# Optimization experiments

Measured on AMD Instinct MI355X. Metric: run time of the kernel, lower is better.

The kernel has to match this reference:

```python
import jax, jax.numpy as jnp
import numpy as np

B, W, E, D, F = 128, 64, 256, 256, 4  # batch, window, enc_hidden, dec_hidden, out_feats


def setup_inputs() -> dict:
    key = jax.random.key(0)
    ks = jax.random.split(key, 16)
    s = 0.05
    return {
        "input_encoded": jax.random.normal(ks[0], (B, W, E), jnp.float32),
        "y_history": jax.random.normal(ks[1], (B, W, F), jnp.float32),
        # attn_layer: Linear(2D+E -> E), Tanh, Linear(E -> 1)
        "attn_w1": jax.random.normal(ks[2], (E, 2 * D + E), jnp.float32) * s,
        "attn_b1": jax.random.normal(ks[3], (E,), jnp.float32) * s,
        "attn_w2": jax.random.normal(ks[4], (1, E), jnp.float32) * s,
        "attn_b2": jax.random.normal(ks[5], (1,), jnp.float32) * s,
        # single-layer LSTM cell: input F, hidden D (gate order i,f,g,o)
        "w_ih": jax.random.normal(ks[6], (4 * D, F), jnp.float32) * s,
        "w_hh": jax.random.normal(ks[7], (4 * D, D), jnp.float32) * s,
        "b_ih": jax.random.normal(ks[8], (4 * D,), jnp.float32) * s,
        "b_hh": jax.random.normal(ks[9], (4 * D,), jnp.float32) * s,
        # fc: Linear(E+F -> F) (weights normal_() in torch, scaled here for stability)
        "fc_w": jax.random.normal(ks[10], (F, E + F), jnp.float32) * s,
        "fc_b": jax.random.normal(ks[11], (F,), jnp.float32) * s,
        # fc_final: Linear(D+E -> F)
        "fcf_w": jax.random.normal(ks[12], (F, D + E), jnp.float32) * s,
        "fcf_b": jax.random.normal(ks[13], (F,), jnp.float32) * s,
    }


def _decoder(input_encoded, y_history, attn_w1, attn_b1, attn_w2, attn_b2,
             w_ih, w_hh, b_ih, b_hh, fc_w, fc_b, fcf_w, fcf_b):
    b = input_encoded.shape[0]
    h0 = jnp.zeros((b, D), input_encoded.dtype)
    c0 = jnp.zeros((b, D), input_encoded.dtype)
    ctx0 = jnp.zeros((b, E), input_encoded.dtype)
    y_seq = jnp.transpose(y_history, (1, 0, 2))  # [W, B, F]

    def step(carry, y_t):
        h, c, _ = carry  # h, c: [B, D]
        # additive attention over encoder timesteps
        hc = jnp.broadcast_to(h[:, None, :], (b, W, D))
        cc = jnp.broadcast_to(c[:, None, :], (b, W, D))
        x = jnp.concatenate([hc, cc, input_encoded], axis=2)  # [B, W, 2D+E]
        z = jnp.tanh(jnp.einsum('bwk,ek->bwe', x, attn_w1) + attn_b1)
        scores = jnp.einsum('bwe,oe->bwo', z, attn_w2)[..., 0] + attn_b2[0]  # [B, W]
        attn = jax.nn.softmax(scores, axis=1)
        context = jnp.einsum('bw,bwe->be', attn, input_encoded)  # [B, E]
        # fc over (context, y_t)
        y_tilde = jnp.concatenate([context, y_t], axis=1) @ fc_w.T + fc_b  # [B, F]
        # one LSTM cell step (torch gate order: i, f, g, o)
        gates = y_tilde @ w_ih.T + b_ih + h @ w_hh.T + b_hh  # [B, 4D]
        i_g, f_g, g_g, o_g = jnp.split(gates, 4, axis=1)
        c_new = jax.nn.sigmoid(f_g) * c + jax.nn.sigmoid(i_g) * jnp.tanh(g_g)
        h_new = jax.nn.sigmoid(o_g) * jnp.tanh(c_new)
        return (h_new, c_new, context), None

    (h, c, context), _ = jax.lax.scan(step, (h0, c0, ctx0), y_seq)
    return jnp.concatenate([h, context], axis=1) @ fcf_w.T + fcf_b  # [B, F]


def reference(input_encoded, y_history, attn_w1, attn_b1, attn_w2, attn_b2,
              w_ih, w_hh, b_ih, b_hh, fc_w, fc_b, fcf_w, fcf_b):
    return _decoder(input_encoded, y_history, attn_w1, attn_b1, attn_w2, attn_b2,
                    w_ih, w_hh, b_ih, b_hh, fc_w, fc_b, fcf_w, fcf_b)
```

## Files before the change

kernel.cpp:

```cpp
#include <hip/hip_runtime.h>

#define Bn 128
#define Wn 64

typedef _Float16 h2 __attribute__((ext_vector_type(2)));

__device__ unsigned g_f2[256];
__device__ unsigned g_state2[256][2][128];
__device__ unsigned g_ep16[Bn * Wn * 128];
__device__ float4 g_encfc[Bn * Wn];
__device__ float4 g_encfcf[Bn * Wn];
__device__ uint4 g_w1q[32 * 512];
__device__ uint4 g_whq[2 * 32 * 512];

__device__ __forceinline__ float ftanh(float x) {
  float p = __builtin_exp2f(x * 2.885390081777927f);
  return 1.0f - 2.0f * __builtin_amdgcn_rcpf(p + 1.0f);
}
__device__ __forceinline__ float fsigm(float x) {
  float p = __builtin_exp2f(-x * 1.4426950408889634f);
  return __builtin_amdgcn_rcpf(1.0f + p);
}
__device__ __forceinline__ float dot4(float4 a, float4 b) {
  return a.x * b.x + a.y * b.y + a.z * b.z + a.w * b.w;
}
__device__ __forceinline__ float fd2(unsigned w, unsigned h, float acc) {
  h2 a = __builtin_bit_cast(h2, w), b = __builtin_bit_cast(h2, h);
#if __has_builtin(__builtin_amdgcn_fdot2)
  return __builtin_amdgcn_fdot2(a, b, acc, false);
#else
  return acc + (float)a.x * (float)b.x + (float)a.y * (float)b.y;
#endif
}
__device__ __forceinline__ float fd2x4u(uint4 w, uint4 h, float acc) {
  acc = fd2(w.x, h.x, acc);
  acc = fd2(w.y, h.y, acc);
  acc = fd2(w.z, h.z, acc);
  acc = fd2(w.w, h.w, acc);
  return acc;
}
__device__ __forceinline__ unsigned pk(float a, float b) {
  h2 h = {(_Float16)a, (_Float16)b};
  return __builtin_bit_cast(unsigned, h);
}
__device__ __forceinline__ void ast(unsigned* p, unsigned v) {
  __hip_atomic_store(p, v, __ATOMIC_RELAXED, __HIP_MEMORY_SCOPE_AGENT);
}
__device__ __forceinline__ unsigned ald(unsigned* p) {
  return __hip_atomic_load(p, __ATOMIC_RELAXED, __HIP_MEMORY_SCOPE_AGENT);
}

__global__ void reset_kernel(float* out) {
  int t = threadIdx.x;
  if (t < 256) g_f2[t] = 0u;
  if (t < 512) out[t] = 0.f;
}

__global__ __launch_bounds__(256) void pack_kernel(const float* __restrict__ w1,
                                                   const float* __restrict__ w_hh) {
  int idx = blockIdx.x * 256 + threadIdx.x;
  const float* src;
  uint4* dst;
  if (idx < 32 * 512) {
    int i = idx >> 9, t = idx & 511;
    int e = t >> 1, kh = t & 1;
    int col = (i < 16) ? (kh * 128 + 8 * i) : (256 + kh * 128 + 8 * (i - 16));
    src = w1 + (size_t)e * 768 + col;
    dst = g_w1q + idx;
  } else {
    int j = idx - 32 * 512;
    int p = j >> 14, rem = j & 16383, i = rem >> 9, t = rem & 511;
    int q = t >> 7, dl = t & 127;
    int row = q * 256 + 128 * p + dl;
    src = w_hh + (size_t)row * 256 + 8 * i;
    dst = g_whq + j;
  }
  uint4 o;
  o.x = pk(src[0], src[1]); o.y = pk(src[2], src[3]);
  o.z = pk(src[4], src[5]); o.w = pk(src[6], src[7]);
  *dst = o;
}

__global__ __launch_bounds__(256) void eproj_kernel(const float* __restrict__ enc,
                                                    const float* __restrict__ w1,
                                                    const float* __restrict__ b1) {
  __shared__ __align__(16) float4 encs[16][64];
  __shared__ float accs[16][256];
  const int m0 = blockIdx.x * 16;
  const int tid = threadIdx.x;
  const float4* eg = (const float4*)(enc + (size_t)m0 * 256);
#pragma unroll
  for (int i = 0; i < 4; i++) {
    int idx = tid + 256 * i;
    encs[idx >> 6][idx & 63] = eg[idx];
  }
  __syncthreads();
  const int e = tid;
  float acc[16];
#pragma unroll
  for (int i = 0; i < 16; i++) acc[i] = 0.f;
  const float4* wrow = (const float4*)(w1 + e * 768 + 512);
  for (int k4 = 0; k4 < 64; k4++) {
    float4 wv = wrow[k4];
#pragma unroll
    for (int i = 0; i < 16; i++) acc[i] += dot4(wv, encs[i][k4]);
  }
  float bb = b1[e];
#pragma unroll
  for (int i = 0; i < 16; i++) accs[i][e] = acc[i] + bb;
  __syncthreads();
#pragma unroll
  for (int r = 0; r < 8; r++) {
    int idx = r * 256 + tid;
    int i = idx >> 7, jp = idx & 127;
    g_ep16[(size_t)(m0 + i) * 128 + jp] = pk(accs[i][2 * jp], accs[i][2 * jp + 1]);
  }
}

__global__ __launch_bounds__(256) void encfc_kernel(const float* __restrict__ enc,
                                                    const float* __restrict__ fc_w,
                                                    const float* __restrict__ fcf_w) {
  __shared__ __align__(16) float4 encs[16][64];
  const int m0 = blockIdx.x * 16;
  const int tid = threadIdx.x;
  const float4* eg = (const float4*)(enc + (size_t)m0 * 256);
#pragma unroll
  for (int i = 0; i < 4; i++) {
    int idx = tid + 256 * i;
    encs[idx >> 6][idx & 63] = eg[idx];
  }
  __syncthreads();
  if (tid < 128) {
    const int r = tid >> 3, o = tid & 7;
    const float* wr = (o < 4) ? (fc_w + o * 260) : (fcf_w + (o - 4) * 512 + 256);
    const float4* w4 = (const float4*)wr;
    float a = 0.f;
#pragma unroll 8
    for (int k = 0; k < 64; k++) a += dot4(w4[k], encs[r][k]);
    if (o < 4) ((float*)&g_encfc[m0 + r])[o] = a;
    else ((float*)&g_encfcf[m0 + r])[o - 4] = a;
  }
}

__global__ __launch_bounds__(512) void decoder_kernel(
    const float* __restrict__ yhist, const float* __restrict__ w2,
    const float* __restrict__ w_ih, const float* __restrict__ b_ih,
    const float* __restrict__ b_hh,
    const float* __restrict__ fc_w, const float* __restrict__ fc_b,
    const float* __restrict__ fcf_w, const float* __restrict__ fcf_b,
    float* __restrict__ out) {
  __shared__ __align__(16) unsigned st_l[256];
  __shared__ float hcp_l[256];
  __shared__ float att_l[64];
  __shared__ float ag_l[512];
  __shared__ float w2_l[256];
  __shared__ unsigned ep_l[64 * 132];
  __shared__ __align__(16) float4 yh_l[64];
  __shared__ float fcy_l[16];
  __shared__ float fcb_l[4];

  const int g = blockIdx.x, tid = threadIdx.x;
  const int b = g & 127, p = g >> 7, other = g ^ 128;
  const int l = tid & 63, wv = tid >> 6;

  const int kh = tid & 1, e_own = tid >> 1;
  const int q = tid >> 7, dl = tid & 127;
  const int grow = q * 256 + 128 * p + dl;
  const float4 wih = *(const float4*)(w_ih + (size_t)grow * 4);
  const float bs = b_ih[grow] + b_hh[grow];
  const float4 efc = g_encfc[b * 64 + l];

  const uint4* w1base = g_w1q + tid;
  const uint4* whbase = g_whq + (p << 14) + tid;

  if (tid < 256) { st_l[tid] = 0u; w2_l[tid] = w2[tid]; }
  if (tid < 64) yh_l[tid] = ((const float4*)yhist)[b * 64 + tid];
  if (tid < 16) fcy_l[tid] = fc_w[(tid >> 2) * 260 + 256 + (tid & 3)];
  if (tid < 4) fcb_l[tid] = fc_b[tid];
#pragma unroll
  for (int i = 0; i < 16; i++) {
    int idx = tid + 512 * i;
    int w = idx >> 7, u = idx & 127;
    ep_l[w * 132 + u] = g_ep16[(size_t)(b * 64 + w) * 128 + u];
  }
  float c0 = 0.f, c1 = 0.f;
  __syncthreads();

  float attw = 0.f;
  const uint4* stq = (const uint4*)st_l;
  for (int t = 0; t < Wn; t++) {
    {
      float a = 0.f;
#pragma unroll
      for (int i = 0; i < 16; i++) a = fd2x4u(w1base[i * 512], stq[kh * 16 + i], a);
#pragma unroll
      for (int i = 0; i < 16; i++) a = fd2x4u(w1base[(16 + i) * 512], stq[32 + kh * 16 + i], a);
      a += __shfl_xor(a, 1, 64);
      if (kh == 0) hcp_l[e_own] = a;
    }
    __syncthreads();
    {
      const int w = tid >> 3, j = tid & 7;
      const unsigned* ep = &ep_l[w * 132 + j * 16];
      const float* hp = &hcp_l[32 * j];
      const float* vv = &w2_l[32 * j];
      float s = 0.f;
#pragma unroll
      for (int i = 0; i < 4; i++) {
        uint4 u = *(const uint4*)(ep + 4 * i);
        float4 h0 = *(const float4*)(hp + 8 * i);
        float4 h1 = *(const float4*)(hp + 8 * i + 4);
        float4 v0 = *(const float4*)(vv + 8 * i);
        float4 v1 = *(const float4*)(vv + 8 * i + 4);
        h2 aa;
        aa = __builtin_bit_cast(h2, u.x);
        s += v0.x * ftanh((float)aa.x + h0.x) + v0.y * ftanh((float)aa.y + h0.y);
        aa = __builtin_bit_cast(h2, u.y);
        s += v0.z * ftanh((float)aa.x + h0.z) + v0.w * ftanh((float)aa.y + h0.w);
        aa = __builtin_bit_cast(h2, u.z);
        s += v1.x * ftanh((float)aa.x + h1.x) + v1.y * ftanh((float)aa.y + h1.y);
        aa = __builtin_bit_cast(h2, u.w);
        s += v1.z * ftanh((float)aa.x + h1.z) + v1.w * ftanh((float)aa.y + h1.w);
      }
      s += __shfl_xor(s, 1, 64);
      s += __shfl_xor(s, 2, 64);
      s += __shfl_xor(s, 4, 64);
      if (j == 0) att_l[w] = s;
    }
    __syncthreads();
    {
      float sc = att_l[l];
      float m = sc;
#pragma unroll
      for (int dd = 32; dd; dd >>= 1) m = fmaxf(m, __shfl_xor(m, dd, 64));
      float pr = __builtin_exp2f((sc - m) * 1.4426950408889634f);
      float su = pr;
#pragma unroll
      for (int dd = 32; dd; dd >>= 1) su += __shfl_xor(su, dd, 64);
      attw = pr * __builtin_amdgcn_rcpf(su);
    }
    float4 yt4;
    {
      float rx = attw * efc.x, ry = attw * efc.y, rz = attw * efc.z, rw = attw * efc.w;
#pragma unroll
      for (int dd = 32; dd; dd >>= 1) {
        rx += __shfl_xor(rx, dd, 64);
        ry += __shfl_xor(ry, dd, 64);
        rz += __shfl_xor(rz, dd, 64);
        rw += __shfl_xor(rw, dd, 64);
      }
      float4 yv = yh_l[t];
      yt4.x = rx + fcb_l[0] + fcy_l[0] * yv.x + fcy_l[1] * yv.y + fcy_l[2] * yv.z + fcy_l[3] * yv.w;
      yt4.y = ry + fcb_l[1] + fcy_l[4] * yv.x + fcy_l[5] * yv.y + fcy_l[6] * yv.z + fcy_l[7] * yv.w;
      yt4.z = rz + fcb_l[2] + fcy_l[8] * yv.x + fcy_l[9] * yv.y + fcy_l[10] * yv.z + fcy_l[11] * yv.w;
      yt4.w = rw + fcb_l[3] + fcy_l[12] * yv.x + fcy_l[13] * yv.y + fcy_l[14] * yv.z + fcy_l[15] * yv.w;
    }
    {
      float aA = bs + dot4(wih, yt4);
#pragma unroll
      for (int i = 0; i < 32; i++) aA = fd2x4u(whbase[i * 512], stq[i], aA);
      ag_l[q * 128 + dl] = aA;
    }
    __syncthreads();
    if (wv == 0) {
      const int d0 = 2 * l, d1 = d0 + 1;
      float i0 = fsigm(ag_l[d0]), i1 = fsigm(ag_l[d1]);
      float f0 = fsigm(ag_l[128 + d0]), f1 = fsigm(ag_l[128 + d1]);
      float G0 = ftanh(ag_l[256 + d0]), G1 = ftanh(ag_l[256 + d1]);
      float o0 = fsigm(ag_l[384 + d0]), o1 = fsigm(ag_l[384 + d1]);
      float cn0 = f0 * c0 + i0 * G0, cn1 = f1 * c1 + i1 * G1;
      float hn0 = o0 * ftanh(cn0), hn1 = o1 * ftanh(cn1);
      c0 = cn0; c1 = cn1;
      unsigned hp = pk(hn0, hn1), cp = pk(cn0, cn1);
      st_l[64 * p + l] = hp;
      st_l[128 + 64 * p + l] = cp;
      if (t < 63) {
        ast(&g_state2[g][t & 1][l], hp);
        ast(&g_state2[g][t & 1][64 + l], cp);
        asm volatile("s_waitcnt vmcnt(0)" ::: "memory");
        if (l == 0) ast(&g_f2[g], (unsigned)(t + 1));
      }
    } else if (wv == 4 && t < 63) {
      while ((int)ald(&g_f2[other]) < t + 1) __builtin_amdgcn_s_sleep(4);
      asm volatile("" ::: "memory");
      unsigned hp = ald(&g_state2[other][t & 1][l]);
      unsigned cp = ald(&g_state2[other][t & 1][64 + l]);
      st_l[64 * (1 - p) + l] = hp;
      st_l[128 + 64 * (1 - p) + l] = cp;
    }
    __syncthreads();
  }

  if (wv < 4) {
    const int f = wv;
    h2 hh = __builtin_bit_cast(h2, st_l[64 * p + l]);
    float v = fcf_w[f * 512 + 128 * p + 2 * l] * (float)hh.x +
              fcf_w[f * 512 + 128 * p + 2 * l + 1] * (float)hh.y;
    if (p == 0) {
      float4 fv = g_encfcf[b * 64 + l];
      v += attw * ((const float*)&fv)[f];
    }
#pragma unroll
    for (int dd = 32; dd; dd >>= 1) v += __shfl_xor(v, dd, 64);
    if (l == 0) atomicAdd(out + b * 4 + f, v + ((p == 0) ? fcf_b[f] : 0.f));
  }
}

extern "C" void kernel_launch(void* const* d_in, const int* in_sizes, int n_in,
                              void* d_out, int out_size, void* d_ws, size_t ws_size,
                              hipStream_t stream) {
  (void)in_sizes; (void)n_in; (void)d_ws; (void)ws_size; (void)out_size;
  const float* enc   = (const float*)d_in[0];
  const float* yhist = (const float*)d_in[1];
  const float* w1    = (const float*)d_in[2];
  const float* b1    = (const float*)d_in[3];
  const float* w2    = (const float*)d_in[4];
  const float* w_ih  = (const float*)d_in[6];
  const float* w_hh  = (const float*)d_in[7];
  const float* b_ih  = (const float*)d_in[8];
  const float* b_hh  = (const float*)d_in[9];
  const float* fc_w  = (const float*)d_in[10];
  const float* fc_b  = (const float*)d_in[11];
  const float* fcf_w = (const float*)d_in[12];
  const float* fcf_b = (const float*)d_in[13];
  float* out = (float*)d_out;

  reset_kernel<<<dim3(1), dim3(512), 0, stream>>>(out);
  pack_kernel<<<dim3(192), dim3(256), 0, stream>>>(w1, w_hh);
  eproj_kernel<<<dim3(512), dim3(256), 0, stream>>>(enc, w1, b1);
  encfc_kernel<<<dim3(512), dim3(256), 0, stream>>>(enc, fc_w, fcf_w);
  decoder_kernel<<<dim3(256), dim3(512), 0, stream>>>(yhist, w2, w_ih, b_ih, b_hh,
                                                      fc_w, fc_b, fcf_w, fcf_b, out);
}
```

Baseline: 708.5 us.

## Split recurrent matvecs by input half and stream weights via LDS DMA pipeline

Each of the two cooperating blocks per batch row now computes partial products over only its own half of the h/c state, for all attention rows and all gate rows. It exchanges partial sums (hcp and gate partials) through global memory instead of exchanging the state itself. Weights are repacked into a per-wave stream and fed through a triple-buffered global_load_lds DMA pipeline, so the L2 weight loads overlap the fdot2 compute. The attention score layout is also reworked, and the cross-block exchange payload grows from 128 to 768 words per step, which adds traffic and extra barriers on the critical path.

```diff
diff --git a/kernel.cpp b/kernel.cpp
--- a/kernel.cpp
+++ b/kernel.cpp
@@ -5,13 +5,12 @@
 
 typedef _Float16 h2 __attribute__((ext_vector_type(2)));
 
-__device__ unsigned g_f2[256];
-__device__ unsigned g_state2[256][2][128];
+__device__ unsigned g_flag[256];
+__device__ unsigned g_post[256][2][768];
 __device__ unsigned g_ep16[Bn * Wn * 128];
 __device__ float4 g_encfc[Bn * Wn];
 __device__ float4 g_encfcf[Bn * Wn];
-__device__ uint4 g_w1q[32 * 512];
-__device__ uint4 g_whq[2 * 32 * 512];
+__device__ uint4 g_wstream[2 * 24576];
 
 __device__ __forceinline__ float ftanh(float x) {
   float p = __builtin_exp2f(x * 2.885390081777927f);
@@ -52,33 +51,36 @@
 
 __global__ void reset_kernel(float* out) {
   int t = threadIdx.x;
-  if (t < 256) g_f2[t] = 0u;
+  if (t < 256) g_flag[t] = 0u;
   if (t < 512) out[t] = 0.f;
 }
 
 __global__ __launch_bounds__(256) void pack_kernel(const float* __restrict__ w1,
                                                    const float* __restrict__ w_hh) {
   int idx = blockIdx.x * 256 + threadIdx.x;
+  int p = idx / 24576;
+  int LIN = idx % 24576;
+  int l = LIN & 63;
+  int t2 = LIN >> 6;
+  int ii = t2 & 3;
+  int t3 = t2 >> 2;
+  int w = t3 / 12;
+  int s = t3 - 12 * w;
   const float* src;
-  uint4* dst;
-  if (idx < 32 * 512) {
-    int i = idx >> 9, t = idx & 511;
-    int e = t >> 1, kh = t & 1;
-    int col = (i < 16) ? (kh * 128 + 8 * i) : (256 + kh * 128 + 8 * (i - 16));
-    src = w1 + (size_t)e * 768 + col;
-    dst = g_w1q + idx;
+  if (s < 4) {
+    int E = w * 32 + s * 8 + (l >> 3);
+    int u = (l & 7) + 8 * ii;
+    int col = (u < 16) ? (128 * p + 8 * u) : (256 + 128 * p + 8 * (u - 16));
+    src = w1 + (size_t)E * 768 + col;
   } else {
-    int j = idx - 32 * 512;
-    int p = j >> 14, rem = j & 16383, i = rem >> 9, t = rem & 511;
-    int q = t >> 7, dl = t & 127;
-    int row = q * 256 + 128 * p + dl;
-    src = w_hh + (size_t)row * 256 + 8 * i;
-    dst = g_whq + j;
+    int R = w * 128 + (s - 4) * 16 + (l >> 2);
+    int u = (l & 3) + 4 * ii;
+    src = w_hh + (size_t)R * 256 + 128 * p + 8 * u;
   }
   uint4 o;
   o.x = pk(src[0], src[1]); o.y = pk(src[2], src[3]);
   o.z = pk(src[4], src[5]); o.w = pk(src[6], src[7]);
-  *dst = o;
+  g_wstream[idx] = o;
 }
 
 __global__ __launch_bounds__(256) void eproj_kernel(const float* __restrict__ enc,
@@ -142,38 +144,83 @@
   }
 }
 
-__global__ __launch_bounds__(512) void decoder_kernel(
+#define AS1C(pp) ((const __attribute__((address_space(1))) void*)(pp))
+#define AS3C(pp) ((__attribute__((address_space(3))) void*)(pp))
+
+#define DMAISSUE(s) do {                                                                   \
+    __builtin_amdgcn_global_load_lds(AS1C(gsrc + (s) * 256 + 0 * 64),                      \
+                                     AS3C(&sbuf[wid][(s) % 3][0][0]), 16, 0, 0);           \
+    __builtin_amdgcn_global_load_lds(AS1C(gsrc + (s) * 256 + 1 * 64),                      \
+                                     AS3C(&sbuf[wid][(s) % 3][1][0]), 16, 0, 0);           \
+    __builtin_amdgcn_global_load_lds(AS1C(gsrc + (s) * 256 + 2 * 64),                      \
+                                     AS3C(&sbuf[wid][(s) % 3][2][0]), 16, 0, 0);           \
+    __builtin_amdgcn_global_load_lds(AS1C(gsrc + (s) * 256 + 3 * 64),                      \
+                                     AS3C(&sbuf[wid][(s) % 3][3][0]), 16, 0, 0);           \
+  } while (0)
+
+#define WAITVM(n) do { asm volatile("s_waitcnt vmcnt(" #n ")" ::: "memory");               \
+                       __builtin_amdgcn_sched_barrier(0); } while (0)
+#define WAITLG    do { asm volatile("s_waitcnt lgkmcnt(0)" ::: "memory");                  \
+                       __builtin_amdgcn_sched_barrier(0); } while (0)
+
+#define CONS_W1(s) do {                                                                    \
+    float acc = 0.f;                                                                       \
+    { uint4 wv = sbuf[wid][(s) % 3][0][l]; acc = fd2x4u(wv, stq[(l & 7) + 0], acc); }      \
+    { uint4 wv = sbuf[wid][(s) % 3][1][l]; acc = fd2x4u(wv, stq[(l & 7) + 8], acc); }      \
+    { uint4 wv = sbuf[wid][(s) % 3][2][l]; acc = fd2x4u(wv, stq[(l & 7) + 16], acc); }     \
+    { uint4 wv = sbuf[wid][(s) % 3][3][l]; acc = fd2x4u(wv, stq[(l & 7) + 24], acc); }     \
+    acc += __shfl_xor(acc, 1, 64);                                                         \
+    acc += __shfl_xor(acc, 2, 64);                                                         \
+    acc += __shfl_xor(acc, 4, 64);                                                         \
+    if ((l & 7) == 0) hcp_par[wid * 32 + (s) * 8 + (l >> 3)] = acc;                        \
+  } while (0)
+
+#define CONS_WH(s) do {                                                                    \
+    float acc = 0.f;                                                                       \
+    { uint4 wv = sbuf[wid][(s) % 3][0][l]; acc = fd2x4u(wv, stq[(l & 3) + 0], acc); }      \
+    { uint4 wv = sbuf[wid][(s) % 3][1][l]; acc = fd2x4u(wv, stq[(l & 3) + 4], acc); }      \
+    { uint4 wv = sbuf[wid][(s) % 3][2][l]; acc = fd2x4u(wv, stq[(l & 3) + 8], acc); }      \
+    { uint4 wv = sbuf[wid][(s) % 3][3][l]; acc = fd2x4u(wv, stq[(l & 3) + 12], acc); }     \
+    acc += __shfl_xor(acc, 1, 64);                                                         \
+    acc += __shfl_xor(acc, 2, 64);                                                         \
+    if ((l & 3) == 0) gate_par[wid * 128 + ((s) - 4) * 16 + (l >> 2)] = acc;               \
+  } while (0)
+
+__global__ __launch_bounds__(512, 2) void decoder_kernel(
     const float* __restrict__ yhist, const float* __restrict__ w2,
     const float* __restrict__ w_ih, const float* __restrict__ b_ih,
     const float* __restrict__ b_hh,
     const float* __restrict__ fc_w, const float* __restrict__ fc_b,
     const float* __restrict__ fcf_w, const float* __restrict__ fcf_b,
     float* __restrict__ out) {
-  __shared__ __align__(16) unsigned st_l[256];
-  __shared__ float hcp_l[256];
-  __shared__ float att_l[64];
-  __shared__ float ag_l[512];
+  __shared__ __align__(16) uint4 sbuf[8][3][4][64];
+  __shared__ __align__(16) unsigned st_l[128];
+  __shared__ float hcp_par[256], hcp_in[256];
+  __shared__ __align__(16) float gate_par[1024];
+  __shared__ __align__(16) float gpar_in[512];
+  __shared__ float att_par[8][64];
+  __shared__ float att_w[64];
+  __shared__ __align__(16) float ytil[4];
+  __shared__ unsigned ep_l[64 * 129];
+  __shared__ __align__(16) float4 yh_l[64];
   __shared__ float w2_l[256];
-  __shared__ unsigned ep_l[64 * 132];
-  __shared__ __align__(16) float4 yh_l[64];
   __shared__ float fcy_l[16];
   __shared__ float fcb_l[4];
 
   const int g = blockIdx.x, tid = threadIdx.x;
   const int b = g & 127, p = g >> 7, other = g ^ 128;
-  const int l = tid & 63, wv = tid >> 6;
-
-  const int kh = tid & 1, e_own = tid >> 1;
+  const int wid = tid >> 6, l = tid & 63;
+
   const int q = tid >> 7, dl = tid & 127;
-  const int grow = q * 256 + 128 * p + dl;
-  const float4 wih = *(const float4*)(w_ih + (size_t)grow * 4);
-  const float bs = b_ih[grow] + b_hh[grow];
+  const int R = q * 256 + 128 * p + dl;
+  const float4 wih = *(const float4*)(w_ih + (size_t)R * 4);
+  const float bs = b_ih[R] + b_hh[R];
   const float4 efc = g_encfc[b * 64 + l];
 
-  const uint4* w1base = g_w1q + tid;
-  const uint4* whbase = g_whq + (p << 14) + tid;
-
-  if (tid < 256) { st_l[tid] = 0u; w2_l[tid] = w2[tid]; }
+  const uint4* gsrc = g_wstream + (size_t)p * 24576 + (size_t)wid * 3072 + l;
+
+  if (tid < 128) st_l[tid] = 0u;
+  if (tid < 256) w2_l[tid] = w2[tid];
   if (tid < 64) yh_l[tid] = ((const float4*)yhist)[b * 64 + tid];
   if (tid < 16) fcy_l[tid] = fc_w[(tid >> 2) * 260 + 256 + (tid & 3)];
   if (tid < 4) fcb_l[tid] = fc_b[tid];
@@ -181,55 +228,76 @@
   for (int i = 0; i < 16; i++) {
     int idx = tid + 512 * i;
     int w = idx >> 7, u = idx & 127;
-    ep_l[w * 132 + u] = g_ep16[(size_t)(b * 64 + w) * 128 + u];
+    ep_l[w * 129 + u] = g_ep16[(size_t)(b * 64 + w) * 128 + u];
   }
   float c0 = 0.f, c1 = 0.f;
   __syncthreads();
 
-  float attw = 0.f;
   const uint4* stq = (const uint4*)st_l;
+
   for (int t = 0; t < Wn; t++) {
+    DMAISSUE(0); DMAISSUE(1); DMAISSUE(2);
+    WAITVM(8); CONS_W1(0); WAITLG; DMAISSUE(3);
+    WAITVM(8); CONS_W1(1); WAITLG; DMAISSUE(4);
+    WAITVM(8); CONS_W1(2); WAITLG; DMAISSUE(5);
+    WAITVM(8); CONS_W1(3); WAITLG; DMAISSUE(6);
+    WAITVM(8); CONS_WH(4); WAITLG; DMAISSUE(7);
+    WAITVM(8); CONS_WH(5); WAITLG; DMAISSUE(8);
+    WAITVM(8); CONS_WH(6); WAITLG; DMAISSUE(9);
+    WAITVM(8); CONS_WH(7); WAITLG; DMAISSUE(10);
+    WAITVM(8); CONS_WH(8); WAITLG; DMAISSUE(11);
+    WAITVM(8); CONS_WH(9);
+    WAITVM(4); CONS_WH(10);
+    WAITVM(0); CONS_WH(11);
+    __syncthreads();
+
+    const int tb = t & 1;
+    if (wid == 0) {
+      unsigned* dst = &g_post[g][tb][0];
+      const int j1 = 4 * l, j2 = 4 * l + 256;
+      const int R1 = (j1 >> 7) * 256 + 128 * (1 - p) + (j1 & 127);
+      const int R2 = (j2 >> 7) * 256 + 128 * (1 - p) + (j2 & 127);
+#pragma unroll
+      for (int k = 0; k < 4; k++) ast(dst + 4 * l + k, __builtin_bit_cast(unsigned, hcp_par[4 * l + k]));
+#pragma unroll
+      for (int k = 0; k < 4; k++) ast(dst + 256 + 4 * l + k, __builtin_bit_cast(unsigned, gate_par[R1 + k]));
+#pragma unroll
+      for (int k = 0; k < 4; k++) ast(dst + 512 + 4 * l + k, __builtin_bit_cast(unsigned, gate_par[R2 + k]));
+      asm volatile("s_waitcnt vmcnt(0)" ::: "memory");
+      if (l == 0) ast(&g_flag[g], (unsigned)(t + 1));
+    } else if (wid == 1) {
+      while ((int)ald(&g_flag[other]) < t + 1) __builtin_amdgcn_s_sleep(2);
+      asm volatile("" ::: "memory");
+      unsigned* src = &g_post[other][tb][0];
+#pragma unroll
+      for (int k = 0; k < 4; k++) hcp_in[4 * l + k] = __builtin_bit_cast(float, ald(src + 4 * l + k));
+#pragma unroll
+      for (int k = 0; k < 4; k++) gpar_in[4 * l + k] = __builtin_bit_cast(float, ald(src + 256 + 4 * l + k));
+#pragma unroll
+      for (int k = 0; k < 4; k++) gpar_in[256 + 4 * l + k] = __builtin_bit_cast(float, ald(src + 512 + 4 * l + k));
+    }
+    __syncthreads();
+
     {
-      float a = 0.f;
-#pragma unroll
-      for (int i = 0; i < 16; i++) a = fd2x4u(w1base[i * 512], stq[kh * 16 + i], a);
-#pragma unroll
-      for (int i = 0; i < 16; i++) a = fd2x4u(w1base[(16 + i) * 512], stq[32 + kh * 16 + i], a);
-      a += __shfl_xor(a, 1, 64);
-      if (kh == 0) hcp_l[e_own] = a;
-    }
-    __syncthreads();
-    {
-      const int w = tid >> 3, j = tid & 7;
-      const unsigned* ep = &ep_l[w * 132 + j * 16];
-      const float* hp = &hcp_l[32 * j];
-      const float* vv = &w2_l[32 * j];
-      float s = 0.f;
-#pragma unroll
-      for (int i = 0; i < 4; i++) {
-        uint4 u = *(const uint4*)(ep + 4 * i);
-        float4 h0 = *(const float4*)(hp + 8 * i);
-        float4 h1 = *(const float4*)(hp + 8 * i + 4);
-        float4 v0 = *(const float4*)(vv + 8 * i);
-        float4 v1 = *(const float4*)(vv + 8 * i + 4);
-        h2 aa;
-        aa = __builtin_bit_cast(h2, u.x);
-        s += v0.x * ftanh((float)aa.x + h0.x) + v0.y * ftanh((float)aa.y + h0.y);
-        aa = __builtin_bit_cast(h2, u.y);
-        s += v0.z * ftanh((float)aa.x + h0.z) + v0.w * ftanh((float)aa.y + h0.w);
-        aa = __builtin_bit_cast(h2, u.z);
-        s += v1.x * ftanh((float)aa.x + h1.x) + v1.y * ftanh((float)aa.y + h1.y);
-        aa = __builtin_bit_cast(h2, u.w);
-        s += v1.z * ftanh((float)aa.x + h1.z) + v1.w * ftanh((float)aa.y + h1.w);
+      const unsigned* eprow = &ep_l[l * 129 + wid * 16];
+      float s_acc = 0.f;
+#pragma unroll
+      for (int i = 0; i < 16; i++) {
+        int e0 = 2 * (wid * 16 + i);
+        h2 aa = __builtin_bit_cast(h2, eprow[i]);
+        float hc0 = hcp_par[e0] + hcp_in[e0];
+        float hc1 = hcp_par[e0 + 1] + hcp_in[e0 + 1];
+        s_acc += w2_l[e0] * ftanh((float)aa.x + hc0);
+        s_acc += w2_l[e0 + 1] * ftanh((float)aa.y + hc1);
       }
-      s += __shfl_xor(s, 1, 64);
-      s += __shfl_xor(s, 2, 64);
-      s += __shfl_xor(s, 4, 64);
-      if (j == 0) att_l[w] = s;
-    }
-    __syncthreads();
-    {
-      float sc = att_l[l];
+      att_par[wid][l] = s_acc;
+    }
+    __syncthreads();
+
+    if (wid == 0) {
+      float sc = 0.f;
+#pragma unroll
+      for (int k = 0; k < 8; k++) sc += att_par[k][l];
       float m = sc;
 #pragma unroll
       for (int dd = 32; dd; dd >>= 1) m = fmaxf(m, __shfl_xor(m, dd, 64));
@@ -237,11 +305,9 @@
       float su = pr;
 #pragma unroll
       for (int dd = 32; dd; dd >>= 1) su += __shfl_xor(su, dd, 64);
-      attw = pr * __builtin_amdgcn_rcpf(su);
-    }
-    float4 yt4;
-    {
-      float rx = attw * efc.x, ry = attw * efc.y, rz = attw * efc.z, rw = attw * efc.w;
+      float aw = pr * __builtin_amdgcn_rcpf(su);
+      att_w[l] = aw;
+      float rx = aw * efc.x, ry = aw * efc.y, rz = aw * efc.z, rw = aw * efc.w;
 #pragma unroll
       for (int dd = 32; dd; dd >>= 1) {
         rx += __shfl_xor(rx, dd, 64);
@@ -249,56 +315,46 @@
         rz += __shfl_xor(rz, dd, 64);
         rw += __shfl_xor(rw, dd, 64);
       }
-      float4 yv = yh_l[t];
-      yt4.x = rx + fcb_l[0] + fcy_l[0] * yv.x + fcy_l[1] * yv.y + fcy_l[2] * yv.z + fcy_l[3] * yv.w;
-      yt4.y = ry + fcb_l[1] + fcy_l[4] * yv.x + fcy_l[5] * yv.y + fcy_l[6] * yv.z + fcy_l[7] * yv.w;
-      yt4.z = rz + fcb_l[2] + fcy_l[8] * yv.x + fcy_l[9] * yv.y + fcy_l[10] * yv.z + fcy_l[11] * yv.w;
-      yt4.w = rw + fcb_l[3] + fcy_l[12] * yv.x + fcy_l[13] * yv.y + fcy_l[14] * yv.z + fcy_l[15] * yv.w;
-    }
+      if (l == 0) {
+        float4 yv = yh_l[t];
+        ytil[0] = rx + fcb_l[0] + fcy_l[0] * yv.x + fcy_l[1] * yv.y + fcy_l[2] * yv.z + fcy_l[3] * yv.w;
+        ytil[1] = ry + fcb_l[1] + fcy_l[4] * yv.x + fcy_l[5] * yv.y + fcy_l[6] * yv.z + fcy_l[7] * yv.w;
+        ytil[2] = rz + fcb_l[2] + fcy_l[8] * yv.x + fcy_l[9] * yv.y + fcy_l[10] * yv.z + fcy_l[11] * yv.w;
+        ytil[3] = rw + fcb_l[3] + fcy_l[12] * yv.x + fcy_l[13] * yv.y + fcy_l[14] * yv.z + fcy_l[15] * yv.w;
+      }
+    }
+    __syncthreads();
+
     {
-      float aA = bs + dot4(wih, yt4);
-#pragma unroll
-      for (int i = 0; i < 32; i++) aA = fd2x4u(whbase[i * 512], stq[i], aA);
-      ag_l[q * 128 + dl] = aA;
-    }
-    __syncthreads();
-    if (wv == 0) {
-      const int d0 = 2 * l, d1 = d0 + 1;
-      float i0 = fsigm(ag_l[d0]), i1 = fsigm(ag_l[d1]);
-      float f0 = fsigm(ag_l[128 + d0]), f1 = fsigm(ag_l[128 + d1]);
-      float G0 = ftanh(ag_l[256 + d0]), G1 = ftanh(ag_l[256 + d1]);
-      float o0 = fsigm(ag_l[384 + d0]), o1 = fsigm(ag_l[384 + d1]);
+      float4 yt4 = *(const float4*)ytil;
+      float val = bs + dot4(wih, yt4) + gate_par[R] + gpar_in[tid];
+      gpar_in[tid] = val;
+    }
+    __syncthreads();
+
+    if (tid < 64) {
+      const int d0 = 2 * tid, d1 = d0 + 1;
+      float i0 = fsigm(gpar_in[d0]), i1 = fsigm(gpar_in[d1]);
+      float f0 = fsigm(gpar_in[128 + d0]), f1 = fsigm(gpar_in[128 + d1]);
+      float G0 = ftanh(gpar_in[256 + d0]), G1 = ftanh(gpar_in[256 + d1]);
+      float o0 = fsigm(gpar_in[384 + d0]), o1 = fsigm(gpar_in[384 + d1]);
       float cn0 = f0 * c0 + i0 * G0, cn1 = f1 * c1 + i1 * G1;
       float hn0 = o0 * ftanh(cn0), hn1 = o1 * ftanh(cn1);
       c0 = cn0; c1 = cn1;
-      unsigned hp = pk(hn0, hn1), cp = pk(cn0, cn1);
-      st_l[64 * p + l] = hp;
-      st_l[128 + 64 * p + l] = cp;
-      if (t < 63) {
-        ast(&g_state2[g][t & 1][l], hp);
-        ast(&g_state2[g][t & 1][64 + l], cp);
-        asm volatile("s_waitcnt vmcnt(0)" ::: "memory");
-        if (l == 0) ast(&g_f2[g], (unsigned)(t + 1));
-      }
-    } else if (wv == 4 && t < 63) {
-      while ((int)ald(&g_f2[other]) < t + 1) __builtin_amdgcn_s_sleep(4);
-      asm volatile("" ::: "memory");
-      unsigned hp = ald(&g_state2[other][t & 1][l]);
-      unsigned cp = ald(&g_state2[other][t & 1][64 + l]);
-      st_l[64 * (1 - p) + l] = hp;
-      st_l[128 + 64 * (1 - p) + l] = cp;
-    }
-    __syncthreads();
-  }
-
-  if (wv < 4) {
-    const int f = wv;
-    h2 hh = __builtin_bit_cast(h2, st_l[64 * p + l]);
+      st_l[tid] = pk(hn0, hn1);
+      st_l[64 + tid] = pk(cn0, cn1);
+    }
+    __syncthreads();
+  }
+
+  if (wid < 4) {
+    const int f = wid;
+    h2 hh = __builtin_bit_cast(h2, st_l[l]);
     float v = fcf_w[f * 512 + 128 * p + 2 * l] * (float)hh.x +
               fcf_w[f * 512 + 128 * p + 2 * l + 1] * (float)hh.y;
     if (p == 0) {
       float4 fv = g_encfcf[b * 64 + l];
-      v += attw * ((const float*)&fv)[f];
+      v += att_w[l] * ((const float*)&fv)[f];
     }
 #pragma unroll
     for (int dd = 32; dd; dd >>= 1) v += __shfl_xor(v, dd, 64);
```

After: 845.3 us. 1.19x slower.

## Split attention projection across paired blocks and cache W1 slice in LDS

Applied to the files above, without the earlier changes.

Each of the two paired blocks now computes half of the attention hidden units (128 of 256 E outputs), holding its packed W1 slice in shared memory instead of streaming it from global memory every step. Partial attention scores are exchanged through a second global flag/buffer handshake and summed before the softmax. The W_hh recurrent matvec is started before the score exchange, with its first loads issued early, so it overlaps the inter-block wait. This halves per-block attention work and global weight traffic, at the cost of an extra cross-block synchronisation per timestep.

```diff
diff --git a/kernel.cpp b/kernel.cpp
--- a/kernel.cpp
+++ b/kernel.cpp
@@ -5,13 +5,15 @@
 
 typedef _Float16 h2 __attribute__((ext_vector_type(2)));
 
+__device__ unsigned g_f1[256];
 __device__ unsigned g_f2[256];
+__device__ unsigned g_sc[256][2][64];
 __device__ unsigned g_state2[256][2][128];
 __device__ unsigned g_ep16[Bn * Wn * 128];
 __device__ float4 g_encfc[Bn * Wn];
 __device__ float4 g_encfcf[Bn * Wn];
-__device__ uint4 g_w1q[32 * 512];
-__device__ uint4 g_whq[2 * 32 * 512];
+__device__ uint4 g_w1p[2 * 16 * 512];
+__device__ uint4 g_whp[2 * 32 * 512];
 
 __device__ __forceinline__ float ftanh(float x) {
   float p = __builtin_exp2f(x * 2.885390081777927f);
@@ -52,7 +54,7 @@
 
 __global__ void reset_kernel(float* out) {
   int t = threadIdx.x;
-  if (t < 256) g_f2[t] = 0u;
+  if (t < 256) { g_f1[t] = 0u; g_f2[t] = 0u; }
   if (t < 512) out[t] = 0.f;
 }
 
@@ -61,19 +63,18 @@
   int idx = blockIdx.x * 256 + threadIdx.x;
   const float* src;
   uint4* dst;
-  if (idx < 32 * 512) {
-    int i = idx >> 9, t = idx & 511;
-    int e = t >> 1, kh = t & 1;
-    int col = (i < 16) ? (kh * 128 + 8 * i) : (256 + kh * 128 + 8 * (i - 16));
-    src = w1 + (size_t)e * 768 + col;
-    dst = g_w1q + idx;
+  if (idx < 16384) {
+    int p = idx >> 13, rem = idx & 8191, i = rem >> 9, t = rem & 511;
+    int e = 128 * p + (t >> 2), kq = t & 3;
+    src = w1 + (size_t)e * 768 + kq * 128 + 8 * i;
+    dst = g_w1p + idx;
   } else {
-    int j = idx - 32 * 512;
+    int j = idx - 16384;
     int p = j >> 14, rem = j & 16383, i = rem >> 9, t = rem & 511;
     int q = t >> 7, dl = t & 127;
-    int row = q * 256 + 128 * p + dl;
-    src = w_hh + (size_t)row * 256 + 8 * i;
-    dst = g_whq + j;
+    int R = q * 256 + 128 * p + dl;
+    src = w_hh + (size_t)R * 256 + 8 * i;
+    dst = g_whp + j;
   }
   uint4 o;
   o.x = pk(src[0], src[1]); o.y = pk(src[2], src[3]);
@@ -149,12 +150,13 @@
     const float* __restrict__ fc_w, const float* __restrict__ fc_b,
     const float* __restrict__ fcf_w, const float* __restrict__ fcf_b,
     float* __restrict__ out) {
+  __shared__ __align__(16) uint4 w1l[16][512];
+  __shared__ unsigned ep_l[64 * 66];
   __shared__ __align__(16) unsigned st_l[256];
-  __shared__ float hcp_l[256];
-  __shared__ float att_l[64];
+  __shared__ float hcp_l[128];
+  __shared__ float att_par[64], att_in[64];
   __shared__ float ag_l[512];
-  __shared__ float w2_l[256];
-  __shared__ unsigned ep_l[64 * 132];
+  __shared__ float w2_l[128];
   __shared__ __align__(16) float4 yh_l[64];
   __shared__ float fcy_l[16];
   __shared__ float fcb_l[4];
@@ -163,73 +165,86 @@
   const int b = g & 127, p = g >> 7, other = g ^ 128;
   const int l = tid & 63, wv = tid >> 6;
 
-  const int kh = tid & 1, e_own = tid >> 1;
+  const int kq = tid & 3, e1 = tid >> 2;
   const int q = tid >> 7, dl = tid & 127;
-  const int grow = q * 256 + 128 * p + dl;
-  const float4 wih = *(const float4*)(w_ih + (size_t)grow * 4);
-  const float bs = b_ih[grow] + b_hh[grow];
+  const int R = q * 256 + 128 * p + dl;
+  const float4 wih = *(const float4*)(w_ih + (size_t)R * 4);
+  const float bs = b_ih[R] + b_hh[R];
   const float4 efc = g_encfc[b * 64 + l];
 
-  const uint4* w1base = g_w1q + tid;
-  const uint4* whbase = g_whq + (p << 14) + tid;
-
-  if (tid < 256) { st_l[tid] = 0u; w2_l[tid] = w2[tid]; }
+  const uint4* whp = g_whp + (p << 14) + tid;
+
+  if (tid < 256) st_l[tid] = 0u;
+  if (tid < 128) w2_l[tid] = w2[128 * p + tid];
   if (tid < 64) yh_l[tid] = ((const float4*)yhist)[b * 64 + tid];
   if (tid < 16) fcy_l[tid] = fc_w[(tid >> 2) * 260 + 256 + (tid & 3)];
   if (tid < 4) fcb_l[tid] = fc_b[tid];
 #pragma unroll
-  for (int i = 0; i < 16; i++) {
+  for (int i = 0; i < 8; i++) {
     int idx = tid + 512 * i;
-    int w = idx >> 7, u = idx & 127;
-    ep_l[w * 132 + u] = g_ep16[(size_t)(b * 64 + w) * 128 + u];
-  }
+    int w = idx >> 6, u = idx & 63;
+    ep_l[w * 66 + u] = g_ep16[(size_t)(b * 64 + w) * 128 + 64 * p + u];
+  }
+#pragma unroll
+  for (int i = 0; i < 16; i++) w1l[i][tid] = g_w1p[(p << 13) + (i << 9) + tid];
   float c0 = 0.f, c1 = 0.f;
   __syncthreads();
 
   float attw = 0.f;
   const uint4* stq = (const uint4*)st_l;
   for (int t = 0; t < Wn; t++) {
+    const int tb = t & 1;
+    const unsigned want = (unsigned)(t + 1);
+    uint4 wpre0 = whp[0 * 512], wpre1 = whp[1 * 512];
+    uint4 wpre2 = whp[2 * 512], wpre3 = whp[3 * 512];
     {
       float a = 0.f;
 #pragma unroll
-      for (int i = 0; i < 16; i++) a = fd2x4u(w1base[i * 512], stq[kh * 16 + i], a);
-#pragma unroll
-      for (int i = 0; i < 16; i++) a = fd2x4u(w1base[(16 + i) * 512], stq[32 + kh * 16 + i], a);
+      for (int i = 0; i < 16; i++) a = fd2x4u(w1l[i][tid], stq[kq * 16 + i], a);
       a += __shfl_xor(a, 1, 64);
-      if (kh == 0) hcp_l[e_own] = a;
+      a += __shfl_xor(a, 2, 64);
+      if (kq == 0) hcp_l[e1] = a;
     }
     __syncthreads();
     {
       const int w = tid >> 3, j = tid & 7;
-      const unsigned* ep = &ep_l[w * 132 + j * 16];
-      const float* hp = &hcp_l[32 * j];
-      const float* vv = &w2_l[32 * j];
+      const unsigned* ep = &ep_l[w * 66 + j * 8];
       float s = 0.f;
 #pragma unroll
-      for (int i = 0; i < 4; i++) {
-        uint4 u = *(const uint4*)(ep + 4 * i);
-        float4 h0 = *(const float4*)(hp + 8 * i);
-        float4 h1 = *(const float4*)(hp + 8 * i + 4);
-        float4 v0 = *(const float4*)(vv + 8 * i);
-        float4 v1 = *(const float4*)(vv + 8 * i + 4);
-        h2 aa;
-        aa = __builtin_bit_cast(h2, u.x);
-        s += v0.x * ftanh((float)aa.x + h0.x) + v0.y * ftanh((float)aa.y + h0.y);
-        aa = __builtin_bit_cast(h2, u.y);
-        s += v0.z * ftanh((float)aa.x + h0.z) + v0.w * ftanh((float)aa.y + h0.w);
-        aa = __builtin_bit_cast(h2, u.z);
-        s += v1.x * ftanh((float)aa.x + h1.x) + v1.y * ftanh((float)aa.y + h1.y);
-        aa = __builtin_bit_cast(h2, u.w);
-        s += v1.z * ftanh((float)aa.x + h1.z) + v1.w * ftanh((float)aa.y + h1.w);
+      for (int k = 0; k < 8; k++) {
+        int pi = j * 8 + k;
+        h2 aa = __builtin_bit_cast(h2, ep[k]);
+        s += w2_l[2 * pi] * ftanh((float)aa.x + hcp_l[2 * pi]);
+        s += w2_l[2 * pi + 1] * ftanh((float)aa.y + hcp_l[2 * pi + 1]);
       }
       s += __shfl_xor(s, 1, 64);
       s += __shfl_xor(s, 2, 64);
       s += __shfl_xor(s, 4, 64);
-      if (j == 0) att_l[w] = s;
-    }
-    __syncthreads();
+      if ((tid & 7) == 0) att_par[w] = s;
+    }
+    __syncthreads();
+    if (wv == 0) {
+      ast(&g_sc[g][tb][l], __builtin_bit_cast(unsigned, att_par[l]));
+      asm volatile("s_waitcnt vmcnt(0)" ::: "memory");
+      if (l == 0) ast(&g_f1[g], want);
+    }
+    float aA = bs;
     {
-      float sc = att_l[l];
+      aA = fd2x4u(wpre0, stq[0], aA);
+      aA = fd2x4u(wpre1, stq[1], aA);
+      aA = fd2x4u(wpre2, stq[2], aA);
+      aA = fd2x4u(wpre3, stq[3], aA);
+#pragma unroll
+      for (int i = 4; i < 32; i++) aA = fd2x4u(whp[i * 512], stq[i], aA);
+    }
+    if (wv == 7) {
+      while ((int)ald(&g_f1[other]) < t + 1) __builtin_amdgcn_s_sleep(2);
+      asm volatile("" ::: "memory");
+      att_in[l] = __builtin_bit_cast(float, ald(&g_sc[other][tb][l]));
+    }
+    __syncthreads();
+    {
+      float sc = att_par[l] + att_in[l];
       float m = sc;
 #pragma unroll
       for (int dd = 32; dd; dd >>= 1) m = fmaxf(m, __shfl_xor(m, dd, 64));
@@ -238,9 +253,6 @@
 #pragma unroll
       for (int dd = 32; dd; dd >>= 1) su += __shfl_xor(su, dd, 64);
       attw = pr * __builtin_amdgcn_rcpf(su);
-    }
-    float4 yt4;
-    {
       float rx = attw * efc.x, ry = attw * efc.y, rz = attw * efc.z, rw = attw * efc.w;
 #pragma unroll
       for (int dd = 32; dd; dd >>= 1) {
@@ -250,16 +262,13 @@
         rw += __shfl_xor(rw, dd, 64);
       }
       float4 yv = yh_l[t];
+      float4 yt4;
       yt4.x = rx + fcb_l[0] + fcy_l[0] * yv.x + fcy_l[1] * yv.y + fcy_l[2] * yv.z + fcy_l[3] * yv.w;
       yt4.y = ry + fcb_l[1] + fcy_l[4] * yv.x + fcy_l[5] * yv.y + fcy_l[6] * yv.z + fcy_l[7] * yv.w;
       yt4.z = rz + fcb_l[2] + fcy_l[8] * yv.x + fcy_l[9] * yv.y + fcy_l[10] * yv.z + fcy_l[11] * yv.w;
       yt4.w = rw + fcb_l[3] + fcy_l[12] * yv.x + fcy_l[13] * yv.y + fcy_l[14] * yv.z + fcy_l[15] * yv.w;
-    }
-    {
-      float aA = bs + dot4(wih, yt4);
-#pragma unroll
-      for (int i = 0; i < 32; i++) aA = fd2x4u(whbase[i * 512], stq[i], aA);
-      ag_l[q * 128 + dl] = aA;
+      aA += dot4(wih, yt4);
+      ag_l[tid] = aA;
     }
     __syncthreads();
     if (wv == 0) {
@@ -275,16 +284,16 @@
       st_l[64 * p + l] = hp;
       st_l[128 + 64 * p + l] = cp;
       if (t < 63) {
-        ast(&g_state2[g][t & 1][l], hp);
-        ast(&g_state2[g][t & 1][64 + l], cp);
+        ast(&g_state2[g][tb][l], hp);
+        ast(&g_state2[g][tb][64 + l], cp);
         asm volatile("s_waitcnt vmcnt(0)" ::: "memory");
-        if (l == 0) ast(&g_f2[g], (unsigned)(t + 1));
+        if (l == 0) ast(&g_f2[g], want);
       }
     } else if (wv == 4 && t < 63) {
       while ((int)ald(&g_f2[other]) < t + 1) __builtin_amdgcn_s_sleep(4);
       asm volatile("" ::: "memory");
-      unsigned hp = ald(&g_state2[other][t & 1][l]);
-      unsigned cp = ald(&g_state2[other][t & 1][64 + l]);
+      unsigned hp = ald(&g_state2[other][tb][l]);
+      unsigned cp = ald(&g_state2[other][tb][64 + l]);
       st_l[64 * (1 - p) + l] = hp;
       st_l[128 + 64 * (1 - p) + l] = cp;
     }
```

New measurement: 1.501 ms. +111.8%, slower.
